# Kernel optimization log

Measured on AMD Instinct MI355X. Metric: run time of the kernel, lower is better.

Reference implementation:

```python
import jax, jax.numpy as jnp
import numpy as np

SEQ_LEN = 96      # input window length L
CHANNELS = 7      # enc_in C
FEAT_LEN = 7328   # L + L(L+1)/2 + sum_{i<L} sum_{i<=j<C} (L-j)
PRED_LEN = 720
BATCH = 256


def setup_inputs() -> dict:
    key = jax.random.key(0)
    k_x, k_w, k_b = jax.random.split(key, 3)
    x = jax.random.normal(k_x, (BATCH, SEQ_LEN, CHANNELS), dtype=jnp.float32)
    # nn.Linear(seq_len=7328, pred_len): W [out,in], b [out]
    bound = 1.0 / np.sqrt(FEAT_LEN)
    W = jax.random.uniform(k_w, (PRED_LEN, FEAT_LEN), dtype=jnp.float32, minval=-bound, maxval=bound)
    b = jax.random.uniform(k_b, (PRED_LEN,), dtype=jnp.float32, minval=-bound, maxval=bound)
    return {"x": x, "W": W, "b": b}


def _expand_features(x):
    # Faithful to: temp_2 = einsum('abd,acd->abcd', x, x); temp_3 = einsum('abce,ade->abcde', temp_2, x)
    # then concat of x, temp_2[:, i, i:] for i<L, and temp_3[:, i, j, j:] for i<L, i<=j<C
    # (range(i, C) is empty for i>=C, so only i<C contributes cubic terms).
    # We generate only the consumed triangular slices instead of the dense L^2/L^3 tensors.
    L = x.shape[1]
    C = x.shape[2]
    parts = [x]
    for i in range(L):
        # temp_2[:, i, i:] == x[:, i, :] * x[:, i:, :]   -> [B, L-i, C]
        parts.append(x[:, i:i + 1, :] * x[:, i:, :])
    for i in range(min(L, C)):
        for j in range(i, C):
            # temp_3[:, i, j, j:] == x[:, i] * x[:, j] * x[:, j:, :]  -> [B, L-j, C]
            parts.append(x[:, i:i + 1, :] * x[:, j:j + 1, :] * x[:, j:, :])
    return jnp.concatenate(parts, axis=1)  # [B, FEAT_LEN, C]


def reference(x, W, b):
    feat = _expand_features(x)                       # [B, 7328, C]
    # shared Linear applied along the feature/time axis (permute(0,2,1) -> Linear -> permute back)
    out = jnp.einsum('bsc,ps->bpc', feat, W) + b[None, :, None]  # [B, pred_len, C]
    return out
```

## Files before the change

kernel.cpp:

```cpp
#include <hip/hip_runtime.h>
#include <hip/hip_bf16.h>

#define L 96
#define CH 7
#define K_FEAT 7328
#define KPAD 7360
#define K8 (KPAD / 8)
#define KT64 115
#define Q_END 4752
#define PRED 720
#define NPAD 768
#define BATCH 256
#define M_TOT (BATCH * CH)
#define NSPLIT 6
#define W_BLKS (NPAD * K8 / 256)
#define FEAT_BLKS (BATCH * 4)

typedef __attribute__((ext_vector_type(8))) short bf16x8;
typedef __attribute__((ext_vector_type(4))) float f32x4;

#define SZ_A    ((size_t)M_TOT * KPAD * 2)
#define SZ_W    ((size_t)NPAD * KPAD * 2)
#define SZ_PS   ((size_t)NSPLIT * M_TOT * NPAD * 4)
#define OFF_AH  ((size_t)0)
#define OFF_WH  (OFF_AH + SZ_A)
#define OFF_PS  (OFF_WH + SZ_W)
#define WS_REQ  (OFF_PS + SZ_PS)

static __device__ __forceinline__ unsigned short f2bf(float f) {
    __hip_bfloat16 h = __float2bfloat16(f);
    return *(unsigned short*)&h;
}

static __device__ __forceinline__ void async_cp16(const unsigned short* g, unsigned short* l) {
    __builtin_amdgcn_global_load_lds(
        (const __attribute__((address_space(1))) unsigned int*)g,
        (__attribute__((address_space(3))) unsigned int*)l, 16, 0, 0);
}

static __device__ ushort4 feat_idx(int k) {
    unsigned short t1 = 96, t2 = 96, t3 = 0;
    if (k < L) {
        t3 = (unsigned short)k;
    } else if (k < Q_END) {
        int r = k - L;
        int i = 0, base = 0;
        while (base + (L - i) <= r) { base += L - i; ++i; }
        t2 = (unsigned short)i;
        t3 = (unsigned short)(i + (r - base));
    } else {
        int r = k - Q_END;
        int base = 0;
        for (int i = 0; i < CH; ++i) {
            for (int j = i; j < CH; ++j) {
                int len = L - j;
                if (r < base + len) {
                    return make_ushort4((unsigned short)i, (unsigned short)j,
                                        (unsigned short)(j + (r - base)), 0);
                }
                base += len;
            }
        }
    }
    return make_ushort4(t1, t2, t3, 0);
}

static __device__ __forceinline__ void adv_idx(int& t1, int& t2, int& t3) {
    if (t1 == 96) {
        if (t2 == 96) {
            if (t3 < L - 1) ++t3; else { t2 = 0; t3 = 0; }
        } else {
            if (t3 < L - 1) ++t3;
            else if (t2 < L - 1) { ++t2; t3 = t2; }
            else { t1 = 0; t2 = 0; t3 = 0; }
        }
    } else {
        if (t3 < L - 1) ++t3;
        else if (t2 < CH - 1) { ++t2; t3 = t2; }
        else { ++t1; t2 = t1; t3 = t1; }
    }
}

__global__ __launch_bounds__(256) void prep_all2(
    const float* __restrict__ x, const float* __restrict__ W,
    unsigned short* __restrict__ Ah, unsigned short* __restrict__ Wh) {
    __shared__ float xl[CH][L + 1];
    const int bid = blockIdx.x;
    const int tid = threadIdx.x;

    if (bid < FEAT_BLKS) {
        const int b = bid >> 2;
        const int part = bid & 3;
        for (int i = tid; i < L * CH; i += 256) {
            int t = i / CH, c = i - t * CH;
            xl[c][t] = x[(size_t)b * L * CH + i];
        }
        if (tid < CH) xl[tid][L] = 1.0f;
        __syncthreads();

        const int span = CH * K8 / 4;
        unsigned short* Ab = Ah + (size_t)b * CH * KPAD;
        const int q1 = (part + 1) * span;
        for (int q = part * span + tid; q < q1; q += 256) {
            int c = q / K8, ch8 = q - c * K8;
            int k = ch8 * 8;
            ushort4 e0 = feat_idx(k);
            int t1 = e0.x, t2 = e0.y, t3 = e0.z;
            unsigned short o[8];
            #pragma unroll
            for (int j = 0; j < 8; ++j) {
                int kk = k + j;
                float v = 0.0f;
                if (kk < K_FEAT) v = xl[c][t1] * xl[c][t2] * xl[c][t3];
                o[j] = f2bf(v);
                adv_idx(t1, t2, t3);
            }
            *(uint4*)&Ab[(size_t)c * KPAD + k] = *(uint4*)o;
        }
    } else {
        int gid = (bid - FEAT_BLKS) * 256 + tid;
        int n = gid / K8, ch8 = gid - n * K8;
        int k = ch8 * 8;
        unsigned short o[8];
        #pragma unroll
        for (int j = 0; j < 8; ++j) {
            int kk = k + j;
            float v = (n < PRED && kk < K_FEAT) ? W[(size_t)n * K_FEAT + kk] : 0.0f;
            o[j] = f2bf(v);
        }
        *(uint4*)&Wh[(size_t)n * KPAD + k] = *(uint4*)o;
    }
}

__global__ __launch_bounds__(256, 2) void gemm2(
    const unsigned short* __restrict__ Ah, const unsigned short* __restrict__ Wh,
    float* __restrict__ ps) {
    __shared__ unsigned short S[2][2][128 * 64];

    const int tid = threadIdx.x;
    const int lane = tid & 63;
    const int w = tid >> 6;
    const int wr = w >> 1, wc = w & 1;

    const int id = blockIdx.x;
    const int nid = (id & 7) * 63 + (id >> 3);
    const int bx = nid % 14;
    const int rest = nid / 14;
    const int by = rest % 6;
    const int bz = rest / 6;
    const int m0 = bx * 128;
    const int n0 = by * 128;
    const int kt0 = (KT64 * bz) / NSPLIT;
    const int kt1 = (KT64 * (bz + 1)) / NSPLIT;

    const int cg = (lane & 7) ^ (lane >> 3);
    const unsigned short* gA[4];
    const unsigned short* gW[4];
    #pragma unroll
    for (int q = 0; q < 4; ++q) {
        int row = w * 32 + q * 8 + (lane >> 3);
        gA[q] = Ah + (size_t)(m0 + row) * KPAD + cg * 8 + kt0 * 64;
        gW[q] = Wh + (size_t)(n0 + row) * KPAD + cg * 8 + kt0 * 64;
    }

#define STAGE(B) do { \
        _Pragma("unroll") \
        for (int q = 0; q < 4; ++q) { \
            async_cp16(gA[q], &S[B][0][(w * 256 + q * 64) * 8]); \
            async_cp16(gW[q], &S[B][1][(w * 256 + q * 64) * 8]); \
            gA[q] += 64; gW[q] += 64; \
        } \
    } while (0)

    const int lr = lane & 15;
    const int ck = lane >> 4;
    int offA[4][2], offW[4][2];
    #pragma unroll
    for (int mi = 0; mi < 4; ++mi) {
        int r = wr * 64 + mi * 16 + lr;
        #pragma unroll
        for (int h = 0; h < 2; ++h)
            offA[mi][h] = r * 128 + (((h * 4 + ck) ^ (r & 7)) << 4);
    }
    #pragma unroll
    for (int ni = 0; ni < 4; ++ni) {
        int r = wc * 64 + ni * 16 + lr;
        #pragma unroll
        for (int h = 0; h < 2; ++h)
            offW[ni][h] = r * 128 + (((h * 4 + ck) ^ (r & 7)) << 4);
    }

    f32x4 acc[4][4] = {};

    STAGE(0);
    asm volatile("s_waitcnt vmcnt(0)" ::: "memory");
    __builtin_amdgcn_s_barrier();
    int cur = 0;
    for (int kt = kt0; kt < kt1; ++kt) {
        const bool has_next = (kt + 1 < kt1);
        if (has_next) {
            STAGE(cur ^ 1);
            asm volatile("s_waitcnt vmcnt(8)" ::: "memory");
        } else {
            asm volatile("s_waitcnt vmcnt(0)" ::: "memory");
        }
        __builtin_amdgcn_sched_barrier(0);
        __builtin_amdgcn_s_barrier();
        __builtin_amdgcn_sched_barrier(0);

        const char* baseA = (const char*)S[cur][0];
        const char* baseW = (const char*)S[cur][1];
        bf16x8 ah[4][2], wh[4][2];
        #pragma unroll
        for (int mi = 0; mi < 4; ++mi) {
            ah[mi][0] = *(const bf16x8*)(baseA + offA[mi][0]);
            ah[mi][1] = *(const bf16x8*)(baseA + offA[mi][1]);
        }
        #pragma unroll
        for (int ni = 0; ni < 4; ++ni) {
            wh[ni][0] = *(const bf16x8*)(baseW + offW[ni][0]);
            wh[ni][1] = *(const bf16x8*)(baseW + offW[ni][1]);
        }
        #pragma unroll
        for (int mi = 0; mi < 4; ++mi) {
            #pragma unroll
            for (int ni = 0; ni < 4; ++ni) {
                acc[mi][ni] = __builtin_amdgcn_mfma_f32_16x16x32_bf16(ah[mi][0], wh[ni][0], acc[mi][ni], 0, 0, 0);
                acc[mi][ni] = __builtin_amdgcn_mfma_f32_16x16x32_bf16(ah[mi][1], wh[ni][1], acc[mi][ni], 0, 0, 0);
            }
        }
        __builtin_amdgcn_s_barrier();
        cur ^= 1;
    }
#undef STAGE

    float* pb = ps + (size_t)bz * M_TOT * NPAD;
    #pragma unroll
    for (int mi = 0; mi < 4; ++mi) {
        #pragma unroll
        for (int ni = 0; ni < 4; ++ni) {
            const int n = n0 + wc * 64 + ni * 16 + lr;
            const int mr = m0 + wr * 64 + mi * 16 + ck * 4;
            #pragma unroll
            for (int r = 0; r < 4; ++r) {
                pb[(size_t)(mr + r) * NPAD + n] = acc[mi][ni][r];
            }
        }
    }
}

__global__ __launch_bounds__(256) void reduce_k(
    const float* __restrict__ ps, const float* __restrict__ bias,
    float* __restrict__ out) {
    int gid = blockIdx.x * 256 + threadIdx.x;
    int b = gid / PRED, p = gid - b * PRED;
    float bv = bias[p];
    float o[CH];
    #pragma unroll
    for (int c = 0; c < CH; ++c) o[c] = bv;
    #pragma unroll
    for (int s = 0; s < NSPLIT; ++s) {
        const float* pb = ps + (size_t)s * M_TOT * NPAD + (size_t)b * CH * NPAD + p;
        #pragma unroll
        for (int c = 0; c < CH; ++c) o[c] += pb[(size_t)c * NPAD];
    }
    float* ob = out + (size_t)gid * CH;
    #pragma unroll
    for (int c = 0; c < CH; ++c) ob[c] = o[c];
}

#define BM 64
#define BN 64
#define BK 32
#define XSTRIDE 101

__global__ void build_table(ushort4* __restrict__ tab) {
    int k = blockIdx.x * blockDim.x + threadIdx.x;
    if (k < K_FEAT) tab[k] = feat_idx(k);
}

__global__ __launch_bounds__(256) void fused_poly_gemm(
    const float* __restrict__ x, const float* __restrict__ W,
    const float* __restrict__ bias, const ushort4* __restrict__ tab,
    float* __restrict__ out) {
    __shared__ float xt[BM][XSTRIDE];
    __shared__ float At[BK][BM];
    __shared__ float Wt[BK][BN];

    const int tid = threadIdx.x;
    const int m0 = blockIdx.x * BM;
    const int n0 = blockIdx.y * BN;

    for (int idx = tid; idx < BM * L; idx += 256) {
        int r = idx / L, t = idx - r * L;
        int m = m0 + r;
        int b = m / CH, c = m - b * CH;
        xt[r][t] = x[(b * L + t) * CH + c];
    }
    if (tid < BM) xt[tid][96] = 1.0f;
    __syncthreads();

    const int tm = tid & 15;
    const int tn = tid >> 4;
    float acc[4][4] = {};

    for (int k0 = 0; k0 < K_FEAT; k0 += BK) {
        #pragma unroll
        for (int q = tid; q < 512; q += 256) {
            int n = q >> 3, kq = q & 7;
            float4 wv;
            if (n0 + n < PRED) wv = *(const float4*)&W[(size_t)(n0 + n) * K_FEAT + k0 + kq * 4];
            else wv = make_float4(0.f, 0.f, 0.f, 0.f);
            Wt[kq * 4 + 0][n] = wv.x; Wt[kq * 4 + 1][n] = wv.y;
            Wt[kq * 4 + 2][n] = wv.z; Wt[kq * 4 + 3][n] = wv.w;
        }
        {
            int k = tid >> 3, mg = tid & 7;
            ushort4 e = tab[k0 + k];
            float p[8];
            #pragma unroll
            for (int mm = 0; mm < 8; ++mm) {
                int m = mg * 8 + mm;
                p[mm] = xt[m][e.x] * xt[m][e.y] * xt[m][e.z];
            }
            *(float4*)&At[k][mg * 8]     = make_float4(p[0], p[1], p[2], p[3]);
            *(float4*)&At[k][mg * 8 + 4] = make_float4(p[4], p[5], p[6], p[7]);
        }
        __syncthreads();
        #pragma unroll 8
        for (int k = 0; k < BK; ++k) {
            float4 a = *(const float4*)&At[k][tm * 4];
            float4 wv = *(const float4*)&Wt[k][tn * 4];
            acc[0][0] = fmaf(a.x, wv.x, acc[0][0]); acc[0][1] = fmaf(a.x, wv.y, acc[0][1]);
            acc[0][2] = fmaf(a.x, wv.z, acc[0][2]); acc[0][3] = fmaf(a.x, wv.w, acc[0][3]);
            acc[1][0] = fmaf(a.y, wv.x, acc[1][0]); acc[1][1] = fmaf(a.y, wv.y, acc[1][1]);
            acc[1][2] = fmaf(a.y, wv.z, acc[1][2]); acc[1][3] = fmaf(a.y, wv.w, acc[1][3]);
            acc[2][0] = fmaf(a.z, wv.x, acc[2][0]); acc[2][1] = fmaf(a.z, wv.y, acc[2][1]);
            acc[2][2] = fmaf(a.z, wv.z, acc[2][2]); acc[2][3] = fmaf(a.z, wv.w, acc[2][3]);
            acc[3][0] = fmaf(a.w, wv.x, acc[3][0]); acc[3][1] = fmaf(a.w, wv.y, acc[3][1]);
            acc[3][2] = fmaf(a.w, wv.z, acc[3][2]); acc[3][3] = fmaf(a.w, wv.w, acc[3][3]);
        }
        __syncthreads();
    }
    #pragma unroll
    for (int i = 0; i < 4; ++i) {
        int m = m0 + tm * 4 + i;
        int b = m / CH, c = m - b * CH;
        #pragma unroll
        for (int j = 0; j < 4; ++j) {
            int n = n0 + tn * 4 + j;
            if (n < PRED) out[((size_t)b * PRED + n) * CH + c] = acc[i][j] + bias[n];
        }
    }
}

extern "C" void kernel_launch(void* const* d_in, const int* in_sizes, int n_in,
                              void* d_out, int out_size, void* d_ws, size_t ws_size,
                              hipStream_t stream) {
    const float* x    = (const float*)d_in[0];
    const float* W    = (const float*)d_in[1];
    const float* bias = (const float*)d_in[2];
    float* out = (float*)d_out;
    char* ws = (char*)d_ws;

    if (ws_size >= WS_REQ) {
        unsigned short* Ah = (unsigned short*)(ws + OFF_AH);
        unsigned short* Wh = (unsigned short*)(ws + OFF_WH);
        float* psum = (float*)(ws + OFF_PS);

        hipLaunchKernelGGL(prep_all2, dim3(FEAT_BLKS + W_BLKS), dim3(256), 0, stream,
                           x, W, Ah, Wh);
        hipLaunchKernelGGL(gemm2, dim3(14 * 6 * NSPLIT), dim3(256), 0, stream, Ah, Wh, psum);
        hipLaunchKernelGGL(reduce_k, dim3(BATCH * PRED / 256), dim3(256), 0, stream,
                           psum, bias, out);
    } else {
        ushort4* tab = (ushort4*)ws;
        hipLaunchKernelGGL(build_table, dim3((K_FEAT + 255) / 256), dim3(256), 0, stream, tab);
        dim3 grid(M_TOT / BM, (PRED + BN - 1) / BN);
        hipLaunchKernelGGL(fused_poly_gemm, grid, dim3(256), 0, stream, x, W, bias, tab, out);
    }
}
```

Baseline: 66.09 us.

## Widen GEMM tile to 128x256 with 96KB dynamic LDS and XCD-aware block mapping

Doubles the N dimension of each GEMM block tile from 128 to 256, so each wave computes a 64x128 sub-tile with 32 accumulators and each A tile loaded from global memory feeds twice as many MFMAs. The LDS double buffer grows to 96KB of dynamic shared memory, launch bounds drop to one block per CU, and the grid shrinks from 504 to 252 blocks. Block IDs are remapped so the 8 XCDs get contiguous chunks of 32 or 31 tiles. The aim is less redundant global and LDS traffic per FLOP, at the cost of occupancy, register pressure and fewer blocks than CUs.

```diff
diff --git a/kernel.cpp b/kernel.cpp
--- a/kernel.cpp
+++ b/kernel.cpp
@@ -15,6 +15,7 @@
 #define NSPLIT 6
 #define W_BLKS (NPAD * K8 / 256)
 #define FEAT_BLKS (BATCH * 4)
+#define GEMM_BLKS (14 * 3 * NSPLIT)
 
 typedef __attribute__((ext_vector_type(8))) short bf16x8;
 typedef __attribute__((ext_vector_type(4))) float f32x4;
@@ -132,10 +133,10 @@
     }
 }
 
-__global__ __launch_bounds__(256, 2) void gemm2(
+__global__ __launch_bounds__(256, 1) void gemm4(
     const unsigned short* __restrict__ Ah, const unsigned short* __restrict__ Wh,
     float* __restrict__ ps) {
-    __shared__ unsigned short S[2][2][128 * 64];
+    extern __shared__ unsigned short S[];
 
     const int tid = threadIdx.x;
     const int lane = tid & 63;
@@ -143,38 +144,46 @@
     const int wr = w >> 1, wc = w & 1;
 
     const int id = blockIdx.x;
-    const int nid = (id & 7) * 63 + (id >> 3);
-    const int bx = nid % 14;
-    const int rest = nid / 14;
-    const int by = rest % 6;
-    const int bz = rest / 6;
+    const int xcd = id & 7;
+    const int wgid = (xcd < 4 ? xcd * 32 : 128 + (xcd - 4) * 31) + (id >> 3);
+    const int bx = wgid % 14;
+    const int rest = wgid / 14;
+    const int by = rest % 3;
+    const int bz = rest / 3;
     const int m0 = bx * 128;
-    const int n0 = by * 128;
+    const int n0 = by * 256;
     const int kt0 = (KT64 * bz) / NSPLIT;
     const int kt1 = (KT64 * (bz + 1)) / NSPLIT;
 
     const int cg = (lane & 7) ^ (lane >> 3);
     const unsigned short* gA[4];
-    const unsigned short* gW[4];
+    const unsigned short* gW[8];
     #pragma unroll
     for (int q = 0; q < 4; ++q) {
         int row = w * 32 + q * 8 + (lane >> 3);
         gA[q] = Ah + (size_t)(m0 + row) * KPAD + cg * 8 + kt0 * 64;
+    }
+    #pragma unroll
+    for (int q = 0; q < 8; ++q) {
+        int row = w * 64 + q * 8 + (lane >> 3);
         gW[q] = Wh + (size_t)(n0 + row) * KPAD + cg * 8 + kt0 * 64;
     }
 
 #define STAGE(B) do { \
+        unsigned short* _ba = S + (B) * 24576; \
         _Pragma("unroll") \
         for (int q = 0; q < 4; ++q) { \
-            async_cp16(gA[q], &S[B][0][(w * 256 + q * 64) * 8]); \
-            async_cp16(gW[q], &S[B][1][(w * 256 + q * 64) * 8]); \
-            gA[q] += 64; gW[q] += 64; \
+            async_cp16(gA[q], _ba + w * 2048 + q * 512); gA[q] += 64; \
+        } \
+        _Pragma("unroll") \
+        for (int q = 0; q < 8; ++q) { \
+            async_cp16(gW[q], _ba + 8192 + w * 4096 + q * 512); gW[q] += 64; \
         } \
     } while (0)
 
     const int lr = lane & 15;
     const int ck = lane >> 4;
-    int offA[4][2], offW[4][2];
+    int offA[4][2], offW[8][2];
     #pragma unroll
     for (int mi = 0; mi < 4; ++mi) {
         int r = wr * 64 + mi * 16 + lr;
@@ -183,24 +192,23 @@
             offA[mi][h] = r * 128 + (((h * 4 + ck) ^ (r & 7)) << 4);
     }
     #pragma unroll
-    for (int ni = 0; ni < 4; ++ni) {
-        int r = wc * 64 + ni * 16 + lr;
+    for (int ni = 0; ni < 8; ++ni) {
+        int r = wc * 128 + ni * 16 + lr;
         #pragma unroll
         for (int h = 0; h < 2; ++h)
             offW[ni][h] = r * 128 + (((h * 4 + ck) ^ (r & 7)) << 4);
     }
 
-    f32x4 acc[4][4] = {};
+    f32x4 acc[4][8] = {};
 
     STAGE(0);
     asm volatile("s_waitcnt vmcnt(0)" ::: "memory");
     __builtin_amdgcn_s_barrier();
     int cur = 0;
     for (int kt = kt0; kt < kt1; ++kt) {
-        const bool has_next = (kt + 1 < kt1);
-        if (has_next) {
+        if (kt + 1 < kt1) {
             STAGE(cur ^ 1);
-            asm volatile("s_waitcnt vmcnt(8)" ::: "memory");
+            asm volatile("s_waitcnt vmcnt(12)" ::: "memory");
         } else {
             asm volatile("s_waitcnt vmcnt(0)" ::: "memory");
         }
@@ -208,23 +216,23 @@
         __builtin_amdgcn_s_barrier();
         __builtin_amdgcn_sched_barrier(0);
 
-        const char* baseA = (const char*)S[cur][0];
-        const char* baseW = (const char*)S[cur][1];
-        bf16x8 ah[4][2], wh[4][2];
+        const char* baseA = (const char*)(S + cur * 24576);
+        const char* baseW = baseA + 16384;
+        bf16x8 ah[4][2], wh[8][2];
         #pragma unroll
         for (int mi = 0; mi < 4; ++mi) {
             ah[mi][0] = *(const bf16x8*)(baseA + offA[mi][0]);
             ah[mi][1] = *(const bf16x8*)(baseA + offA[mi][1]);
         }
         #pragma unroll
-        for (int ni = 0; ni < 4; ++ni) {
+        for (int ni = 0; ni < 8; ++ni) {
             wh[ni][0] = *(const bf16x8*)(baseW + offW[ni][0]);
             wh[ni][1] = *(const bf16x8*)(baseW + offW[ni][1]);
         }
         #pragma unroll
         for (int mi = 0; mi < 4; ++mi) {
             #pragma unroll
-            for (int ni = 0; ni < 4; ++ni) {
+            for (int ni = 0; ni < 8; ++ni) {
                 acc[mi][ni] = __builtin_amdgcn_mfma_f32_16x16x32_bf16(ah[mi][0], wh[ni][0], acc[mi][ni], 0, 0, 0);
                 acc[mi][ni] = __builtin_amdgcn_mfma_f32_16x16x32_bf16(ah[mi][1], wh[ni][1], acc[mi][ni], 0, 0, 0);
             }
@@ -238,8 +246,8 @@
     #pragma unroll
     for (int mi = 0; mi < 4; ++mi) {
         #pragma unroll
-        for (int ni = 0; ni < 4; ++ni) {
-            const int n = n0 + wc * 64 + ni * 16 + lr;
+        for (int ni = 0; ni < 8; ++ni) {
+            const int n = n0 + wc * 128 + ni * 16 + lr;
             const int mr = m0 + wr * 64 + mi * 16 + ck * 4;
             #pragma unroll
             for (int r = 0; r < 4; ++r) {
@@ -370,7 +378,8 @@
 
         hipLaunchKernelGGL(prep_all2, dim3(FEAT_BLKS + W_BLKS), dim3(256), 0, stream,
                            x, W, Ah, Wh);
-        hipLaunchKernelGGL(gemm2, dim3(14 * 6 * NSPLIT), dim3(256), 0, stream, Ah, Wh, psum);
+        hipLaunchKernelGGL(gemm4, dim3(GEMM_BLKS), dim3(256), 96 * 1024, stream,
+                           Ah, Wh, psum);
         hipLaunchKernelGGL(reduce_k, dim3(BATCH * PRED / 256), dim3(256), 0, stream,
                            psum, bias, out);
     } else {
```

Result: slower. 68.63 us (+3.8%).
